# Performance work log

Measured on AMD Instinct MI355X. Metric: run time of the kernel, lower is better.

The kernel has to match this reference:

```python
import jax, jax.numpy as jnp
import numpy as np

NUM_BUCKETS = 14
SCALE_FACTOR = 3.0
MAX_SHAPE = (800, 1333)  # (H, W)
SIDE = int(np.ceil(NUM_BUCKETS / 2.0))  # 7
B, N = 8, 131072


def setup_inputs() -> dict:
    key = jax.random.key(0)
    k1, k2, k3, k4, kc, ko = jax.random.split(key, 6)
    # valid xyxy proposals inside a ~1333x800 image
    x1 = jax.random.uniform(k1, (B, N)) * 1000.0
    y1 = jax.random.uniform(k2, (B, N)) * 600.0
    w = jax.random.uniform(k3, (B, N)) * 300.0 + 16.0
    h = jax.random.uniform(k4, (B, N)) * 300.0 + 16.0
    proposals = jnp.stack([x1, y1, x1 + w, y1 + h], axis=-1)
    cls_preds = jax.random.normal(kc, (B, N * 4 * SIDE), dtype=jnp.float32)
    offset_preds = jax.random.normal(ko, (B, N * 4 * SIDE), dtype=jnp.float32) * 0.5
    return {"proposals": proposals, "cls_preds": cls_preds, "offset_preds": offset_preds}


def reference(proposals, cls_preds, offset_preds):
    batch = cls_preds.shape[0]
    cls = cls_preds.reshape(batch, -1, SIDE)                 # [B, 4N, S]
    scores = jax.nn.softmax(cls, axis=2)
    score_topk, score_label = jax.lax.top_k(scores, 2)      # [B, 4N, 2]

    # bbox_rescale: scale w/h about the box center
    cx = (proposals[..., 0] + proposals[..., 2]) * 0.5
    cy = (proposals[..., 1] + proposals[..., 3]) * 0.5
    pw = (proposals[..., 2] - proposals[..., 0]) * SCALE_FACTOR
    ph = (proposals[..., 3] - proposals[..., 1]) * SCALE_FACTOR
    px1 = cx - 0.5 * pw
    py1 = cy - 0.5 * ph
    px2 = cx + 0.5 * pw
    py2 = cy + 0.5 * ph
    bucket_w = pw / NUM_BUCKETS
    bucket_h = ph / NUM_BUCKETS

    # rows are interleaved (l, r, t, d) per proposal
    inds_l = score_label[:, 0::4, 0]
    inds_r = score_label[:, 1::4, 0]
    inds_t = score_label[:, 2::4, 0]
    inds_d = score_label[:, 3::4, 0]

    f32 = jnp.float32
    l_buckets = px1 + (0.5 + inds_l.astype(f32)) * bucket_w
    r_buckets = px2 - (0.5 + inds_r.astype(f32)) * bucket_w
    t_buckets = py1 + (0.5 + inds_t.astype(f32)) * bucket_h
    d_buckets = py2 - (0.5 + inds_d.astype(f32)) * bucket_h

    offsets = offset_preds.reshape(batch, -1, 4, SIDE)       # [B, N, 4, S]
    l_off = jnp.take_along_axis(offsets[:, :, 0, :], inds_l[..., None], axis=2)[..., 0]
    r_off = jnp.take_along_axis(offsets[:, :, 1, :], inds_r[..., None], axis=2)[..., 0]
    t_off = jnp.take_along_axis(offsets[:, :, 2, :], inds_t[..., None], axis=2)[..., 0]
    d_off = jnp.take_along_axis(offsets[:, :, 3, :], inds_d[..., None], axis=2)[..., 0]

    x1 = l_buckets - l_off * bucket_w
    x2 = r_buckets - r_off * bucket_w
    y1 = t_buckets - t_off * bucket_h
    y2 = d_buckets - d_off * bucket_h

    H, W = MAX_SHAPE
    x1 = jnp.clip(x1, 0.0, W - 1)
    y1 = jnp.clip(y1, 0.0, H - 1)
    x2 = jnp.clip(x2, 0.0, W - 1)
    y2 = jnp.clip(y2, 0.0, H - 1)
    bboxes = jnp.stack([x1, y1, x2, y2], axis=-1)            # [B, N, 4]

    loc_conf = score_topk[:, :, 0]
    top2_neighbor = jnp.abs((score_label[:, :, 0] - score_label[:, :, 1]).astype(f32)) - 1.0
    loc_conf = loc_conf + score_topk[:, :, 1] * top2_neighbor
    loc_conf = loc_conf.reshape(batch, -1, 4).mean(axis=2)   # [B, N]
    return bboxes, loc_conf
```

## Files before the change

kernel.cpp:

```cpp
#include <hip/hip_runtime.h>
#include <math.h>


#define TILE 64
#define PAD_ROW 29

typedef float f32x4_v __attribute__((ext_vector_type(4)));

__global__ __launch_bounds__(64) void bucketing_bbox_wave_kernel(
    const float* __restrict__ proposals,
    const float* __restrict__ cls_preds,
    const float* __restrict__ offset_preds,
    float* __restrict__ out_bboxes,
    float* __restrict__ out_conf)
{
    __shared__ float lds[TILE * PAD_ROW];

    const int t = threadIdx.x;
    const size_t base = (size_t)blockIdx.x * TILE;
    const size_t gid = base + t;

    const float4* clsv = reinterpret_cast<const float4*>(cls_preds) + base * 7;
    const float4* offv = reinterpret_cast<const float4*>(offset_preds) + base * 7;
    float4 creg[7], oreg[7];
#pragma unroll
    for (int k = 0; k < 7; ++k) creg[k] = clsv[t + TILE * k];
#pragma unroll
    for (int k = 0; k < 7; ++k) oreg[k] = offv[t + TILE * k];
    float4 pr = reinterpret_cast<const float4*>(proposals)[gid];

    const int p0 = t / 7;
    const int e0 = t - p0 * 7;

    {
        int p = p0, e = e0;
#pragma unroll
        for (int k = 0; k < 7; ++k) {
            int a = p * PAD_ROW + 4 * e;
            lds[a + 0] = creg[k].x;
            lds[a + 1] = creg[k].y;
            lds[a + 2] = creg[k].z;
            lds[a + 3] = creg[k].w;
            p += 9; e += 1;
            if (e >= 7) { e -= 7; p += 1; }
        }
    }
    __syncthreads();

    float cls[28];
    const int rb = t * PAD_ROW;
#pragma unroll
    for (int j = 0; j < 28; ++j) cls[j] = lds[rb + j];
    __syncthreads();

    {
        int p = p0, e = e0;
#pragma unroll
        for (int k = 0; k < 7; ++k) {
            int a = p * PAD_ROW + 4 * e;
            lds[a + 0] = oreg[k].x;
            lds[a + 1] = oreg[k].y;
            lds[a + 2] = oreg[k].z;
            lds[a + 3] = oreg[k].w;
            p += 9; e += 1;
            if (e >= 7) { e -= 7; p += 1; }
        }
    }

    int   lab0s[4];
    float conf_sum = 0.0f;
#pragma unroll
    for (int s = 0; s < 4; ++s) {
        float best0 = cls[s * 7 + 0];
        float best1 = -INFINITY;
        int   lab0 = 0, lab1 = 0;
#pragma unroll
        for (int j = 1; j < 7; ++j) {
            float x = cls[s * 7 + j];
            bool gt0 = x > best0;
            bool gt1 = x > best1;
            best1 = gt0 ? best0 : (gt1 ? x : best1);
            lab1  = gt0 ? lab0  : (gt1 ? j : lab1);
            best0 = gt0 ? x : best0;
            lab0  = gt0 ? j : lab0;
        }
        float sum = 0.0f;
#pragma unroll
        for (int j = 0; j < 7; ++j) sum += __expf(cls[s * 7 + j] - best0);
        float inv = 1.0f / sum;
        float p0s = inv;
        float p1s = __expf(best1 - best0) * inv;

        lab0s[s] = lab0;
        float neighbor = fabsf((float)(lab0 - lab1)) - 1.0f;
        conf_sum += p0s + p1s * neighbor;
    }

    float cx = (pr.x + pr.z) * 0.5f;
    float cy = (pr.y + pr.w) * 0.5f;
    float pw = (pr.z - pr.x) * 3.0f;
    float ph = (pr.w - pr.y) * 3.0f;
    float px1 = cx - 0.5f * pw;
    float px2 = cx + 0.5f * pw;
    float py1 = cy - 0.5f * ph;
    float py2 = cy + 0.5f * ph;
    float bw = pw / 14.0f;
    float bh = ph / 14.0f;

    __syncthreads();

    float osel0 = lds[rb + 0  + lab0s[0]];
    float osel1 = lds[rb + 7  + lab0s[1]];
    float osel2 = lds[rb + 14 + lab0s[2]];
    float osel3 = lds[rb + 21 + lab0s[3]];

    float l_b = px1 + (0.5f + (float)lab0s[0]) * bw;
    float r_b = px2 - (0.5f + (float)lab0s[1]) * bw;
    float t_b = py1 + (0.5f + (float)lab0s[2]) * bh;
    float d_b = py2 - (0.5f + (float)lab0s[3]) * bh;

    float x1 = l_b - osel0 * bw;
    float x2 = r_b - osel1 * bw;
    float y1 = t_b - osel2 * bh;
    float y2 = d_b - osel3 * bh;

    const float Wm = 1332.0f;
    const float Hm = 799.0f;
    x1 = fminf(fmaxf(x1, 0.0f), Wm);
    x2 = fminf(fmaxf(x2, 0.0f), Wm);
    y1 = fminf(fmaxf(y1, 0.0f), Hm);
    y2 = fminf(fmaxf(y2, 0.0f), Hm);

    f32x4_v bb = {x1, y1, x2, y2};
    __builtin_nontemporal_store(bb, reinterpret_cast<f32x4_v*>(out_bboxes) + gid);
    out_conf[gid] = conf_sum * 0.25f;
}

__global__ __launch_bounds__(256) void bucketing_bbox_tail_kernel(
    const float* __restrict__ proposals,
    const float* __restrict__ cls_preds,
    const float* __restrict__ offset_preds,
    float* __restrict__ out_bboxes,
    float* __restrict__ out_conf,
    int start, int total)
{
    int i = start + blockIdx.x * blockDim.x + threadIdx.x;
    if (i >= total) return;

    float4 pr = reinterpret_cast<const float4*>(proposals)[i];
    float cls[28], offs[28];
    {
        const float4* cp = reinterpret_cast<const float4*>(cls_preds + (size_t)i * 28);
        const float4* op = reinterpret_cast<const float4*>(offset_preds + (size_t)i * 28);
#pragma unroll
        for (int k = 0; k < 7; ++k) reinterpret_cast<float4*>(cls)[k] = cp[k];
#pragma unroll
        for (int k = 0; k < 7; ++k) reinterpret_cast<float4*>(offs)[k] = op[k];
    }
    float cx = (pr.x + pr.z) * 0.5f;
    float cy = (pr.y + pr.w) * 0.5f;
    float pw = (pr.z - pr.x) * 3.0f;
    float ph = (pr.w - pr.y) * 3.0f;
    float px1 = cx - 0.5f * pw, px2 = cx + 0.5f * pw;
    float py1 = cy - 0.5f * ph, py2 = cy + 0.5f * ph;
    float bw = pw / 14.0f, bh = ph / 14.0f;

    int lab0s[4]; float offsel[4]; float conf_sum = 0.0f;
#pragma unroll
    for (int s = 0; s < 4; ++s) {
        float best0 = cls[s * 7], best1 = -INFINITY;
        int lab0 = 0, lab1 = 0;
        float osel = offs[s * 7];
#pragma unroll
        for (int j = 1; j < 7; ++j) {
            float x = cls[s * 7 + j], o = offs[s * 7 + j];
            bool gt0 = x > best0, gt1 = x > best1;
            best1 = gt0 ? best0 : (gt1 ? x : best1);
            lab1  = gt0 ? lab0  : (gt1 ? j : lab1);
            best0 = gt0 ? x : best0;
            lab0  = gt0 ? j : lab0;
            osel  = gt0 ? o : osel;
        }
        float sum = 0.0f;
#pragma unroll
        for (int j = 0; j < 7; ++j) sum += __expf(cls[s * 7 + j] - best0);
        float inv = 1.0f / sum;
        lab0s[s] = lab0; offsel[s] = osel;
        conf_sum += inv + __expf(best1 - best0) * inv * (fabsf((float)(lab0 - lab1)) - 1.0f);
    }
    float x1 = px1 + (0.5f + (float)lab0s[0]) * bw - offsel[0] * bw;
    float x2 = px2 - (0.5f + (float)lab0s[1]) * bw - offsel[1] * bw;
    float y1 = py1 + (0.5f + (float)lab0s[2]) * bh - offsel[2] * bh;
    float y2 = py2 - (0.5f + (float)lab0s[3]) * bh - offsel[3] * bh;
    x1 = fminf(fmaxf(x1, 0.0f), 1332.0f);
    x2 = fminf(fmaxf(x2, 0.0f), 1332.0f);
    y1 = fminf(fmaxf(y1, 0.0f), 799.0f);
    y2 = fminf(fmaxf(y2, 0.0f), 799.0f);
    reinterpret_cast<float4*>(out_bboxes)[i] = make_float4(x1, y1, x2, y2);
    out_conf[i] = conf_sum * 0.25f;
}

extern "C" void kernel_launch(void* const* d_in, const int* in_sizes, int n_in,
                              void* d_out, int out_size, void* d_ws, size_t ws_size,
                              hipStream_t stream) {
    const float* proposals    = (const float*)d_in[0];
    const float* cls_preds    = (const float*)d_in[1];
    const float* offset_preds = (const float*)d_in[2];

    int total = in_sizes[0] / 4;

    float* out_bboxes = (float*)d_out;
    float* out_conf   = (float*)d_out + (size_t)total * 4;

    int full_tiles = total / TILE;
    int rem = total - full_tiles * TILE;

    if (full_tiles > 0) {
        bucketing_bbox_wave_kernel<<<full_tiles, TILE, 0, stream>>>(
            proposals, cls_preds, offset_preds, out_bboxes, out_conf);
    }
    if (rem > 0) {
        int start = full_tiles * TILE;
        bucketing_bbox_tail_kernel<<<(rem + 255) / 256, 256, 0, stream>>>(
            proposals, cls_preds, offset_preds, out_bboxes, out_conf, start, total);
    }
}
```

Baseline: 262.3 us.

## Double-buffer tiles with direct global-to-LDS loads across multiple tiles per block

Each single-wave block now processes eight 64-proposal tiles instead of one. Class scores, offsets and proposals are copied from global memory straight into LDS with global_load_lds, into two alternating buffers. The next tile's loads are issued before computing on the current one, with vmcnt waits acting as the barrier. This removes the register staging and LDS transpose stores of the old kernel and overlaps memory latency with compute. The costs are fewer blocks in the grid, reliance on hand-written waitcnt ordering, and possible LDS bank conflicts from the 28-float row stride.

```diff
diff --git a/kernel.cpp b/kernel.cpp
--- a/kernel.cpp
+++ b/kernel.cpp
@@ -2,138 +2,126 @@
 #include <math.h>
 
 
-#define TILE 64
-#define PAD_ROW 29
+#define WTILE 64
+#define ITERS 8
+#define W_CLS 0
+#define W_OFF 1792
+#define W_PRP 3584
+#define W_BUF 3840
 
 typedef float f32x4_v __attribute__((ext_vector_type(4)));
 
-__global__ __launch_bounds__(64) void bucketing_bbox_wave_kernel(
+__device__ __forceinline__ void gl_lds16(const float* g, float* l) {
+    __builtin_amdgcn_global_load_lds(
+        (const __attribute__((address_space(1))) unsigned int*)g,
+        (__attribute__((address_space(3))) unsigned int*)l, 16, 0, 0);
+}
+
+__global__ __launch_bounds__(64) void bucketing_bbox_pipe_kernel(
     const float* __restrict__ proposals,
     const float* __restrict__ cls_preds,
     const float* __restrict__ offset_preds,
     float* __restrict__ out_bboxes,
     float* __restrict__ out_conf)
 {
-    __shared__ float lds[TILE * PAD_ROW];
+    __shared__ float lds[2][W_BUF];
 
     const int t = threadIdx.x;
-    const size_t base = (size_t)blockIdx.x * TILE;
-    const size_t gid = base + t;
-
-    const float4* clsv = reinterpret_cast<const float4*>(cls_preds) + base * 7;
-    const float4* offv = reinterpret_cast<const float4*>(offset_preds) + base * 7;
-    float4 creg[7], oreg[7];
-#pragma unroll
-    for (int k = 0; k < 7; ++k) creg[k] = clsv[t + TILE * k];
-#pragma unroll
-    for (int k = 0; k < 7; ++k) oreg[k] = offv[t + TILE * k];
-    float4 pr = reinterpret_cast<const float4*>(proposals)[gid];
-
-    const int p0 = t / 7;
-    const int e0 = t - p0 * 7;
-
-    {
-        int p = p0, e = e0;
-#pragma unroll
-        for (int k = 0; k < 7; ++k) {
-            int a = p * PAD_ROW + 4 * e;
-            lds[a + 0] = creg[k].x;
-            lds[a + 1] = creg[k].y;
-            lds[a + 2] = creg[k].z;
-            lds[a + 3] = creg[k].w;
-            p += 9; e += 1;
-            if (e >= 7) { e -= 7; p += 1; }
+    const size_t blk0 = (size_t)blockIdx.x * (ITERS * WTILE);
+
+    auto issue_tile = [&](int i, int b) {
+        const size_t pbase = blk0 + (size_t)i * WTILE;
+        const float* cg = cls_preds    + pbase * 28 + t * 4;
+        const float* og = offset_preds + pbase * 28 + t * 4;
+        const float* pg = proposals    + pbase * 4  + t * 4;
+        float* lb = &lds[b][0];
+#pragma unroll
+        for (int c = 0; c < 7; ++c) gl_lds16(cg + c * 256, lb + W_CLS + c * 256);
+#pragma unroll
+        for (int c = 0; c < 7; ++c) gl_lds16(og + c * 256, lb + W_OFF + c * 256);
+        gl_lds16(pg, lb + W_PRP);
+    };
+
+    asm volatile("" ::: "memory");
+    issue_tile(0, 0);
+
+    for (int i = 0; i < ITERS; ++i) {
+        if (i + 1 < ITERS) {
+            asm volatile("" ::: "memory");
+            issue_tile(i + 1, (i + 1) & 1);
+            asm volatile("s_waitcnt vmcnt(15)" ::: "memory");
+        } else {
+            asm volatile("s_waitcnt vmcnt(0)" ::: "memory");
         }
-    }
-    __syncthreads();
-
-    float cls[28];
-    const int rb = t * PAD_ROW;
-#pragma unroll
-    for (int j = 0; j < 28; ++j) cls[j] = lds[rb + j];
-    __syncthreads();
-
-    {
-        int p = p0, e = e0;
-#pragma unroll
-        for (int k = 0; k < 7; ++k) {
-            int a = p * PAD_ROW + 4 * e;
-            lds[a + 0] = oreg[k].x;
-            lds[a + 1] = oreg[k].y;
-            lds[a + 2] = oreg[k].z;
-            lds[a + 3] = oreg[k].w;
-            p += 9; e += 1;
-            if (e >= 7) { e -= 7; p += 1; }
+
+        const float* lb = &lds[i & 1][0];
+
+        float cls[28];
+        const float4* crow = reinterpret_cast<const float4*>(lb + W_CLS + t * 28);
+#pragma unroll
+        for (int k = 0; k < 7; ++k) reinterpret_cast<float4*>(cls)[k] = crow[k];
+        float4 pr = reinterpret_cast<const float4*>(lb + W_PRP)[t];
+
+        int   lab0s[4];
+        float conf_sum = 0.0f;
+#pragma unroll
+        for (int s = 0; s < 4; ++s) {
+            float best0 = cls[s * 7 + 0];
+            float best1 = -INFINITY;
+            int   lab0 = 0, lab1 = 0;
+#pragma unroll
+            for (int j = 1; j < 7; ++j) {
+                float x = cls[s * 7 + j];
+                bool gt0 = x > best0;
+                bool gt1 = x > best1;
+                best1 = gt0 ? best0 : (gt1 ? x : best1);
+                lab1  = gt0 ? lab0  : (gt1 ? j : lab1);
+                best0 = gt0 ? x : best0;
+                lab0  = gt0 ? j : lab0;
+            }
+            float sum = 0.0f;
+#pragma unroll
+            for (int j = 0; j < 7; ++j) sum += __expf(cls[s * 7 + j] - best0);
+            float inv = 1.0f / sum;
+            lab0s[s] = lab0;
+            float neighbor = fabsf((float)(lab0 - lab1)) - 1.0f;
+            conf_sum += inv + __expf(best1 - best0) * inv * neighbor;
         }
-    }
-
-    int   lab0s[4];
-    float conf_sum = 0.0f;
-#pragma unroll
-    for (int s = 0; s < 4; ++s) {
-        float best0 = cls[s * 7 + 0];
-        float best1 = -INFINITY;
-        int   lab0 = 0, lab1 = 0;
-#pragma unroll
-        for (int j = 1; j < 7; ++j) {
-            float x = cls[s * 7 + j];
-            bool gt0 = x > best0;
-            bool gt1 = x > best1;
-            best1 = gt0 ? best0 : (gt1 ? x : best1);
-            lab1  = gt0 ? lab0  : (gt1 ? j : lab1);
-            best0 = gt0 ? x : best0;
-            lab0  = gt0 ? j : lab0;
-        }
-        float sum = 0.0f;
-#pragma unroll
-        for (int j = 0; j < 7; ++j) sum += __expf(cls[s * 7 + j] - best0);
-        float inv = 1.0f / sum;
-        float p0s = inv;
-        float p1s = __expf(best1 - best0) * inv;
-
-        lab0s[s] = lab0;
-        float neighbor = fabsf((float)(lab0 - lab1)) - 1.0f;
-        conf_sum += p0s + p1s * neighbor;
-    }
-
-    float cx = (pr.x + pr.z) * 0.5f;
-    float cy = (pr.y + pr.w) * 0.5f;
-    float pw = (pr.z - pr.x) * 3.0f;
-    float ph = (pr.w - pr.y) * 3.0f;
-    float px1 = cx - 0.5f * pw;
-    float px2 = cx + 0.5f * pw;
-    float py1 = cy - 0.5f * ph;
-    float py2 = cy + 0.5f * ph;
-    float bw = pw / 14.0f;
-    float bh = ph / 14.0f;
-
-    __syncthreads();
-
-    float osel0 = lds[rb + 0  + lab0s[0]];
-    float osel1 = lds[rb + 7  + lab0s[1]];
-    float osel2 = lds[rb + 14 + lab0s[2]];
-    float osel3 = lds[rb + 21 + lab0s[3]];
-
-    float l_b = px1 + (0.5f + (float)lab0s[0]) * bw;
-    float r_b = px2 - (0.5f + (float)lab0s[1]) * bw;
-    float t_b = py1 + (0.5f + (float)lab0s[2]) * bh;
-    float d_b = py2 - (0.5f + (float)lab0s[3]) * bh;
-
-    float x1 = l_b - osel0 * bw;
-    float x2 = r_b - osel1 * bw;
-    float y1 = t_b - osel2 * bh;
-    float y2 = d_b - osel3 * bh;
-
-    const float Wm = 1332.0f;
-    const float Hm = 799.0f;
-    x1 = fminf(fmaxf(x1, 0.0f), Wm);
-    x2 = fminf(fmaxf(x2, 0.0f), Wm);
-    y1 = fminf(fmaxf(y1, 0.0f), Hm);
-    y2 = fminf(fmaxf(y2, 0.0f), Hm);
-
-    f32x4_v bb = {x1, y1, x2, y2};
-    __builtin_nontemporal_store(bb, reinterpret_cast<f32x4_v*>(out_bboxes) + gid);
-    out_conf[gid] = conf_sum * 0.25f;
+
+        const float* orow = lb + W_OFF + t * 28;
+        float osel0 = orow[0  + lab0s[0]];
+        float osel1 = orow[7  + lab0s[1]];
+        float osel2 = orow[14 + lab0s[2]];
+        float osel3 = orow[21 + lab0s[3]];
+
+        float cx = (pr.x + pr.z) * 0.5f;
+        float cy = (pr.y + pr.w) * 0.5f;
+        float pw = (pr.z - pr.x) * 3.0f;
+        float ph = (pr.w - pr.y) * 3.0f;
+        float px1 = cx - 0.5f * pw;
+        float px2 = cx + 0.5f * pw;
+        float py1 = cy - 0.5f * ph;
+        float py2 = cy + 0.5f * ph;
+        float bw = pw / 14.0f;
+        float bh = ph / 14.0f;
+
+        float x1 = px1 + (0.5f + (float)lab0s[0]) * bw - osel0 * bw;
+        float x2 = px2 - (0.5f + (float)lab0s[1]) * bw - osel1 * bw;
+        float y1 = py1 + (0.5f + (float)lab0s[2]) * bh - osel2 * bh;
+        float y2 = py2 - (0.5f + (float)lab0s[3]) * bh - osel3 * bh;
+
+        const float Wm = 1332.0f;
+        const float Hm = 799.0f;
+        x1 = fminf(fmaxf(x1, 0.0f), Wm);
+        x2 = fminf(fmaxf(x2, 0.0f), Wm);
+        y1 = fminf(fmaxf(y1, 0.0f), Hm);
+        y2 = fminf(fmaxf(y2, 0.0f), Hm);
+
+        const size_t gid = blk0 + (size_t)i * WTILE + t;
+        f32x4_v bb = {x1, y1, x2, y2};
+        __builtin_nontemporal_store(bb, reinterpret_cast<f32x4_v*>(out_bboxes) + gid);
+        __builtin_nontemporal_store(conf_sum * 0.25f, out_conf + gid);
+    }
 }
 
 __global__ __launch_bounds__(256) void bucketing_bbox_tail_kernel(
@@ -212,15 +200,16 @@
     float* out_bboxes = (float*)d_out;
     float* out_conf   = (float*)d_out + (size_t)total * 4;
 
-    int full_tiles = total / TILE;
-    int rem = total - full_tiles * TILE;
-
-    if (full_tiles > 0) {
-        bucketing_bbox_wave_kernel<<<full_tiles, TILE, 0, stream>>>(
+    const int per_block = WTILE * ITERS;
+    int full_blocks = total / per_block;
+    int rem = total - full_blocks * per_block;
+
+    if (full_blocks > 0) {
+        bucketing_bbox_pipe_kernel<<<full_blocks, WTILE, 0, stream>>>(
             proposals, cls_preds, offset_preds, out_bboxes, out_conf);
     }
     if (rem > 0) {
-        int start = full_tiles * TILE;
+        int start = full_blocks * per_block;
         bucketing_bbox_tail_kernel<<<(rem + 255) / 256, 256, 0, stream>>>(
             proposals, cls_preds, offset_preds, out_bboxes, out_conf, start, total);
     }
```

New measurement: 271.9 us. 1.04x slower.
